# Kernel tuning notes

Measured on AMD Instinct MI355X. Metric: run time of the kernel, lower is better.

## Reference

```python
import jax, jax.numpy as jnp
import numpy as np

D_K = 64  # module-level constant in source
NEG = -1e9


def setup_inputs() -> dict:
    key = jax.random.key(0)
    k1, k2, k3, k4 = jax.random.split(key, 4)
    B, H, S, D = 4, 16, 2048, 64
    query = jax.random.normal(k1, (B, H, S, D), dtype=jnp.float32)
    key_t = jax.random.normal(k2, (B, H, S, D), dtype=jnp.float32)
    value = jax.random.normal(k3, (B, H, S, D), dtype=jnp.float32)
    mask = jax.random.randint(k4, (B, 1, S, S), 0, 2) == 1  # bool, broadcast over heads
    return {"query": query, "key": key_t, "value": value, "mask": mask}


def reference(query, key, value, mask):
    # scores = QK^T / sqrt(d_k)   [B,H,S,S]
    scores = jnp.einsum("bhqd,bhkd->bhqk", query, key) / jnp.sqrt(jnp.float32(D_K))
    # masked_fill_(mask, -1e9)
    scores = jnp.where(mask, jnp.float32(NEG), scores)
    # non-standard: multiply masked scores by V, then log_softmax over last dim
    out = jnp.einsum("bhqk,bhkd->bhqd", scores, value)  # [B,H,S,d_v]
    return jax.nn.log_softmax(out, axis=-1)
```

## Files before the change

### kernel.cpp

```cpp
#include <hip/hip_runtime.h>
#include <hip/hip_bf16.h>


typedef __attribute__((ext_vector_type(8))) short bf16x8;
typedef __attribute__((ext_vector_type(16))) float f32x16;

#define NEGV (-1e9f)

__device__ inline unsigned cvt_bf16(float f) {
    unsigned u = __builtin_bit_cast(unsigned, f);
    u += 0x7FFFu + ((u >> 16) & 1u);
    return u >> 16;
}
__device__ inline unsigned pk_bf16(float a, float b) {
    return cvt_bf16(a) | (cvt_bf16(b) << 16);
}
__device__ inline unsigned pk_trunc(float a, float b) {
    return __builtin_amdgcn_perm(__builtin_bit_cast(unsigned, b),
                                 __builtin_bit_cast(unsigned, a), 0x07060302u);
}

__global__ __launch_bounds__(256)
void mask_pack(const int* __restrict__ M, unsigned long long* __restrict__ bitT) {
    const int lane = threadIdx.x & 63;
    const int gw   = (blockIdx.x * 256 + threadIdx.x) >> 6;
    const int b    = gw >> 11;
    const int qt   = (gw >> 8) & 7;
    const int q    = gw & 255;
    const size_t mbase = (size_t)gw * 2048;
    unsigned long long* dst = bitT + (size_t)(b * 8 + qt) * 32 * 256 + q;
#pragma unroll 4
    for (int ki = 0; ki < 32; ki++) {
        const int m = M[mbase + ki * 64 + lane];
        const unsigned long long bal = __ballot(m != 0);
        if (lane == 0) dst[ki * 256] = bal;
    }
}

__global__ __launch_bounds__(256, 4)
void attn_kernel(const float* __restrict__ Q, const float* __restrict__ K,
                 const float* __restrict__ V,
                 const unsigned long long* __restrict__ bitT,
                 float* __restrict__ Out) {
    __shared__ __attribute__((aligned(16))) unsigned short sK[2][64 * 72];
    __shared__ __attribute__((aligned(16))) unsigned short sVt[2][64 * 72];

    const int tid  = threadIdx.x;
    const int wave = tid >> 6;
    const int lane = tid & 63;
    const int half = lane >> 5;
    const int l32  = lane & 31;

    const int bid = blockIdx.x;
    const int h   = bid & 15;
    const int qt2 = (bid >> 4) & 15;
    const int b   = bid >> 8;
    const int bh  = b * 16 + h;
    const int q0  = qt2 * 128;
    const int qt  = qt2 >> 1;
    const int qh  = qt2 & 1;

    const float* Qb = Q + (size_t)(bh * 2048 + q0) * 64;
    const float* Kb = K + (size_t)bh * 2048 * 64;
    const float* Vb = V + (size_t)bh * 2048 * 64;
    const unsigned long long* Bt = bitT + (size_t)(b * 8 + qt) * 32 * 256
                                 + qh * 128 + wave * 32 + l32;

    float4 kp[4];
    float  vp[16];
    unsigned long long mw = Bt[0];
    const int krow = tid >> 4, kc4 = tid & 15;
#pragma unroll
    for (int i = 0; i < 4; i++)
        kp[i] = *(const float4*)(Kb + (size_t)(krow + i * 16) * 64 + kc4 * 4);
#pragma unroll
    for (int i = 0; i < 2; i++) {
        const int kb = (wave * 2 + i) * 8;
#pragma unroll
        for (int j = 0; j < 8; j++)
            vp[i * 8 + j] = Vb[(size_t)(kb + j) * 64 + lane];
    }

    bf16x8 qF[4];
    {
        const float* qr = Qb + (size_t)(wave * 32 + l32) * 64 + half * 8;
#pragma unroll
        for (int dk = 0; dk < 4; dk++) {
            const float4 f0 = *(const float4*)(qr + dk * 16);
            const float4 f1 = *(const float4*)(qr + dk * 16 + 4);
            union { bf16x8 v; unsigned u[4]; } t;
            t.u[0] = pk_bf16(f0.x * 0.125f, f0.y * 0.125f);
            t.u[1] = pk_bf16(f0.z * 0.125f, f0.w * 0.125f);
            t.u[2] = pk_bf16(f1.x * 0.125f, f1.y * 0.125f);
            t.u[3] = pk_bf16(f1.z * 0.125f, f1.w * 0.125f);
            qF[dk] = t.v;
        }
    }

    f32x16 Oacc[2];
#pragma unroll
    for (int db = 0; db < 2; db++)
#pragma unroll
        for (int r = 0; r < 16; r++) Oacc[db][r] = 0.f;

    for (int ki = 0; ki < 32; ki++) {
        const int cur = ki & 1;

#pragma unroll
        for (int i = 0; i < 4; i++) {
            uint2 p;
            p.x = pk_trunc(kp[i].x, kp[i].y);
            p.y = pk_trunc(kp[i].z, kp[i].w);
            *(uint2*)&sK[cur][(krow + i * 16) * 72 + kc4 * 4] = p;
        }
#pragma unroll
        for (int i = 0; i < 2; i++) {
            const int kb = (wave * 2 + i) * 8;
            uint4 p4;
            p4.x = pk_trunc(vp[i * 8 + 0], vp[i * 8 + 1]);
            p4.y = pk_trunc(vp[i * 8 + 2], vp[i * 8 + 3]);
            p4.z = pk_trunc(vp[i * 8 + 4], vp[i * 8 + 5]);
            p4.w = pk_trunc(vp[i * 8 + 6], vp[i * 8 + 7]);
            *(uint4*)&sVt[cur][lane * 72 + kb] = p4;
        }

        __syncthreads();

        unsigned long long mwN = 0;
        if (ki < 31) {
            const int kn = (ki + 1) * 64;
            mwN = Bt[(ki + 1) * 256];
#pragma unroll
            for (int i = 0; i < 4; i++)
                kp[i] = *(const float4*)(Kb + (size_t)(kn + krow + i * 16) * 64 + kc4 * 4);
#pragma unroll
            for (int i = 0; i < 2; i++) {
                const int kb = (wave * 2 + i) * 8;
#pragma unroll
                for (int j = 0; j < 8; j++)
                    vp[i * 8 + j] = Vb[(size_t)(kn + kb + j) * 64 + lane];
            }
        }

#pragma unroll
        for (int jk = 0; jk < 2; jk++) {
            bf16x8 aK[4];
#pragma unroll
            for (int dk = 0; dk < 4; dk++)
                aK[dk] = *(const bf16x8*)&sK[cur][(jk * 32 + l32) * 72 + dk * 16 + half * 8];
            bf16x8 bV[2][2];
#pragma unroll
            for (int p = 0; p < 2; p++)
#pragma unroll
                for (int db = 0; db < 2; db++)
                    bV[p][db] = *(const bf16x8*)&sVt[cur][(db * 32 + l32) * 72 + (jk * 2 + p) * 16 + half * 8];

            const unsigned b32 = (unsigned)(mw >> (jk * 32));
            const unsigned bsh = b32 >> (half * 4);

            f32x16 acc;
#pragma unroll
            for (int rg = 0; rg < 4; rg++) {
                const unsigned nib = bsh >> (rg * 8);
                acc[rg * 4 + 0] = (nib & 1u) ? NEGV : 0.f;
                acc[rg * 4 + 1] = (nib & 2u) ? NEGV : 0.f;
                acc[rg * 4 + 2] = (nib & 4u) ? NEGV : 0.f;
                acc[rg * 4 + 3] = (nib & 8u) ? NEGV : 0.f;
            }
#pragma unroll
            for (int dk = 0; dk < 4; dk++)
                acc = __builtin_amdgcn_mfma_f32_32x32x16_bf16(aK[dk], qF[dk], acc, 0, 0, 0);

#pragma unroll
            for (int p = 0; p < 2; p++) {
                const unsigned P0 = pk_trunc(acc[p * 8 + 0], acc[p * 8 + 1]);
                const unsigned P1 = pk_trunc(acc[p * 8 + 2], acc[p * 8 + 3]);
                const unsigned P2 = pk_trunc(acc[p * 8 + 4], acc[p * 8 + 5]);
                const unsigned P3 = pk_trunc(acc[p * 8 + 6], acc[p * 8 + 7]);
                auto r02 = __builtin_amdgcn_permlane32_swap(P0, P2, false, false);
                auto r13 = __builtin_amdgcn_permlane32_swap(P1, P3, false, false);
                union { bf16x8 v; unsigned u[4]; } aS;
                aS.u[0] = (unsigned)r02[0];
                aS.u[1] = (unsigned)r13[0];
                aS.u[2] = (unsigned)r02[1];
                aS.u[3] = (unsigned)r13[1];
#pragma unroll
                for (int db = 0; db < 2; db++)
                    Oacc[db] = __builtin_amdgcn_mfma_f32_32x32x16_bf16(aS.v, bV[p][db], Oacc[db], 0, 0, 0);
            }
        }

        mw = mwN;
    }

    float* Ob = Out + (size_t)bh * 2048 * 64;
#pragma unroll
    for (int r = 0; r < 16; r++) {
        const float v0 = Oacc[0][r], v1 = Oacc[1][r];
        float mx = fmaxf(v0, v1);
#pragma unroll
        for (int off = 1; off < 32; off <<= 1)
            mx = fmaxf(mx, __shfl_xor(mx, off, 64));
        float s = __expf(v0 - mx) + __expf(v1 - mx);
#pragma unroll
        for (int off = 1; off < 32; off <<= 1)
            s += __shfl_xor(s, off, 64);
        const float lse = mx + __logf(s);
        const int qrow = q0 + wave * 32 + (r & 3) + 8 * (r >> 2) + 4 * half;
        Ob[(size_t)qrow * 64 + l32]      = v0 - lse;
        Ob[(size_t)qrow * 64 + 32 + l32] = v1 - lse;
    }
}

extern "C" void kernel_launch(void* const* d_in, const int* in_sizes, int n_in,
                              void* d_out, int out_size, void* d_ws, size_t ws_size,
                              hipStream_t stream) {
    const float* Q = (const float*)d_in[0];
    const float* K = (const float*)d_in[1];
    const float* V = (const float*)d_in[2];
    const int*   M = (const int*)d_in[3];
    float* Out = (float*)d_out;
    unsigned long long* bitT = (unsigned long long*)d_ws;

    mask_pack<<<dim3(2048), dim3(256), 0, stream>>>(M, bitT);
    attn_kernel<<<dim3(1024), dim3(256), 0, stream>>>(Q, K, V, bitT, Out);
}
```

Baseline: 261.5 us.

## Pre-convert K/V to swizzled bf16 and stage tiles via direct global-to-LDS loads

Adds a preconversion kernel that packs the mask bits and also converts K and transposed V to bf16 in an XOR-swizzled layout in workspace. The attention kernel then stages each tile into LDS with global_load_lds instead of loading fp32 into registers and packing in-kernel, and reads LDS with a swizzle in place of padding. This halves the bytes each of the 16 query-tile blocks per head re-reads for K/V and removes the per-iteration convert and LDS store work. The cost is an extra full pass over K and V, plus a workspace-size check that falls back to the old path.

After: 265.9 us. Within noise of the previous version (+1.7%).

```diff
diff --git a/kernel.cpp b/kernel.cpp
--- a/kernel.cpp
+++ b/kernel.cpp
@@ -18,6 +18,226 @@
 __device__ inline unsigned pk_trunc(float a, float b) {
     return __builtin_amdgcn_perm(__builtin_bit_cast(unsigned, b),
                                  __builtin_bit_cast(unsigned, a), 0x07060302u);
+}
+
+#define WS_BIT_OFF  0u
+#define WS_K_OFF    2097152u
+#define WS_V_OFF    18874368u
+#define WS_NEED     35651584ull
+
+__global__ __launch_bounds__(256)
+void preconv(const int* __restrict__ M, const float* __restrict__ K,
+             const float* __restrict__ V, unsigned long long* __restrict__ bitT,
+             unsigned short* __restrict__ Kswz, unsigned short* __restrict__ Vtswz) {
+    const int tid  = threadIdx.x;
+    const int lane = tid & 63;
+    const int wave = tid >> 6;
+    const int bid  = blockIdx.x;
+
+    if (bid < 2048) {
+        const int gw = (bid * 256 + tid) >> 6;
+        const int b  = gw >> 11;
+        const int qt = (gw >> 8) & 7;
+        const int q  = gw & 255;
+        const size_t mbase = (size_t)gw * 2048;
+        unsigned long long* dst = bitT + (size_t)(b * 8 + qt) * 32 * 256 + q;
+#pragma unroll 4
+        for (int ki = 0; ki < 32; ki++) {
+            const int m = M[mbase + ki * 64 + lane];
+            const unsigned long long bal = __ballot(m != 0);
+            if (lane == 0) dst[ki * 256] = bal;
+        }
+    } else if (bid < 6144) {
+        const unsigned g   = (unsigned)(bid - 2048) * 256 + tid;
+        const int b4  = g & 7;
+        const int row = (g >> 3) & 63;
+        const int d0  = (b4 ^ (row & 7)) * 8;
+        const float* src = K + (size_t)(g >> 3) * 64 + d0;
+        const float4 f0 = *(const float4*)(src);
+        const float4 f1 = *(const float4*)(src + 4);
+        uint4 p;
+        p.x = pk_trunc(f0.x, f0.y); p.y = pk_trunc(f0.z, f0.w);
+        p.z = pk_trunc(f1.x, f1.y); p.w = pk_trunc(f1.z, f1.w);
+        *(uint4*)&Kswz[(size_t)g * 8] = p;
+    } else {
+        const int j    = (bid - 6144) * 4 + wave;
+        const int kgrp = j & 7;
+        const int ki   = (j >> 3) & 31;
+        const int bh   = j >> 8;
+        const size_t vbase = ((size_t)(bh * 2048 + ki * 64 + kgrp * 8)) * 64 + lane;
+        float v[8];
+#pragma unroll
+        for (int jj = 0; jj < 8; jj++) v[jj] = V[vbase + jj * 64];
+        uint4 p;
+        p.x = pk_trunc(v[0], v[1]); p.y = pk_trunc(v[2], v[3]);
+        p.z = pk_trunc(v[4], v[5]); p.w = pk_trunc(v[6], v[7]);
+        const size_t chunk = ((size_t)(bh * 32 + ki) * 64 + lane) * 8 + (kgrp ^ (lane & 7));
+        *(uint4*)&Vtswz[chunk * 8] = p;
+    }
+}
+
+__global__ __launch_bounds__(256, 4)
+void attn_fast(const float* __restrict__ Q,
+               const unsigned short* __restrict__ Kswz,
+               const unsigned short* __restrict__ Vtswz,
+               const unsigned long long* __restrict__ bitT,
+               float* __restrict__ Out) {
+    __shared__ __attribute__((aligned(16))) unsigned short sK[2][64 * 64];
+    __shared__ __attribute__((aligned(16))) unsigned short sVt[2][64 * 64];
+
+    const int tid  = threadIdx.x;
+    const int wave = tid >> 6;
+    const int lane = tid & 63;
+    const int half = lane >> 5;
+    const int l32  = lane & 31;
+
+    const int bid = blockIdx.x;
+    const int h   = bid & 15;
+    const int qt2 = (bid >> 4) & 15;
+    const int b   = bid >> 8;
+    const int bh  = b * 16 + h;
+    const int q0  = qt2 * 128;
+    const int qt  = qt2 >> 1;
+    const int qh  = qt2 & 1;
+
+    const float* Qb = Q + (size_t)(bh * 2048 + q0) * 64;
+    const unsigned short* Kt = Kswz  + ((size_t)bh << 17);
+    const unsigned short* Vt = Vtswz + ((size_t)bh << 17);
+    const unsigned long long* Bt = bitT + (size_t)(b * 8 + qt) * 32 * 256
+                                 + qh * 128 + wave * 32 + l32;
+
+    #define STAGE(buf, ki) do {                                                   \
+        const unsigned short* kg_ = Kt + ((ki) << 12) + wave * 1024 + lane * 8;   \
+        const unsigned short* vg_ = Vt + ((ki) << 12) + wave * 1024 + lane * 8;   \
+        unsigned short* ks_ = &sK[buf][wave * 1024];                              \
+        unsigned short* vs_ = &sVt[buf][wave * 1024];                             \
+        __builtin_amdgcn_global_load_lds(                                         \
+            (const __attribute__((address_space(1))) void*)kg_,                   \
+            (__attribute__((address_space(3))) void*)ks_, 16, 0, 0);              \
+        __builtin_amdgcn_global_load_lds(                                         \
+            (const __attribute__((address_space(1))) void*)(kg_ + 512),           \
+            (__attribute__((address_space(3))) void*)(ks_ + 512), 16, 0, 0);      \
+        __builtin_amdgcn_global_load_lds(                                         \
+            (const __attribute__((address_space(1))) void*)vg_,                   \
+            (__attribute__((address_space(3))) void*)vs_, 16, 0, 0);              \
+        __builtin_amdgcn_global_load_lds(                                         \
+            (const __attribute__((address_space(1))) void*)(vg_ + 512),           \
+            (__attribute__((address_space(3))) void*)(vs_ + 512), 16, 0, 0);      \
+    } while (0)
+
+    STAGE(0, 0);
+    unsigned long long mw = Bt[0];
+
+    bf16x8 qF[4];
+    {
+        const float* qr = Qb + (size_t)(wave * 32 + l32) * 64 + half * 8;
+#pragma unroll
+        for (int dk = 0; dk < 4; dk++) {
+            const float4 f0 = *(const float4*)(qr + dk * 16);
+            const float4 f1 = *(const float4*)(qr + dk * 16 + 4);
+            union { bf16x8 v; unsigned u[4]; } t;
+            t.u[0] = pk_bf16(f0.x * 0.125f, f0.y * 0.125f);
+            t.u[1] = pk_bf16(f0.z * 0.125f, f0.w * 0.125f);
+            t.u[2] = pk_bf16(f1.x * 0.125f, f1.y * 0.125f);
+            t.u[3] = pk_bf16(f1.z * 0.125f, f1.w * 0.125f);
+            qF[dk] = t.v;
+        }
+    }
+
+    f32x16 Oacc[2];
+#pragma unroll
+    for (int db = 0; db < 2; db++)
+#pragma unroll
+        for (int r = 0; r < 16; r++) Oacc[db][r] = 0.f;
+
+    __syncthreads();
+
+    const int swz = (l32 & 7) << 4;
+
+    for (int ki = 0; ki < 32; ki++) {
+        const int cur = ki & 1;
+
+        unsigned long long mwN = 0;
+        if (ki < 31) {
+            STAGE(cur ^ 1, ki + 1);
+            mwN = Bt[(ki + 1) * 256];
+        }
+
+        const char* sKc = (const char*)sK[cur];
+        const char* sVc = (const char*)sVt[cur];
+
+#pragma unroll
+        for (int jk = 0; jk < 2; jk++) {
+            bf16x8 aK[4];
+#pragma unroll
+            for (int dk = 0; dk < 4; dk++)
+                aK[dk] = *(const bf16x8*)(sKc +
+                    ((((jk * 32 + l32) * 128) + dk * 32 + half * 16) ^ swz));
+            bf16x8 bV[2][2];
+#pragma unroll
+            for (int p = 0; p < 2; p++)
+#pragma unroll
+                for (int db = 0; db < 2; db++)
+                    bV[p][db] = *(const bf16x8*)(sVc +
+                        ((((db * 32 + l32) * 128) + (jk * 2 + p) * 32 + half * 16) ^ swz));
+
+            const unsigned b32 = (unsigned)(mw >> (jk * 32));
+            const unsigned bsh = b32 >> (half * 4);
+
+            f32x16 acc;
+#pragma unroll
+            for (int rg = 0; rg < 4; rg++) {
+                const unsigned nib = bsh >> (rg * 8);
+                acc[rg * 4 + 0] = (nib & 1u) ? NEGV : 0.f;
+                acc[rg * 4 + 1] = (nib & 2u) ? NEGV : 0.f;
+                acc[rg * 4 + 2] = (nib & 4u) ? NEGV : 0.f;
+                acc[rg * 4 + 3] = (nib & 8u) ? NEGV : 0.f;
+            }
+#pragma unroll
+            for (int dk = 0; dk < 4; dk++)
+                acc = __builtin_amdgcn_mfma_f32_32x32x16_bf16(aK[dk], qF[dk], acc, 0, 0, 0);
+
+#pragma unroll
+            for (int p = 0; p < 2; p++) {
+                const unsigned P0 = pk_trunc(acc[p * 8 + 0], acc[p * 8 + 1]);
+                const unsigned P1 = pk_trunc(acc[p * 8 + 2], acc[p * 8 + 3]);
+                const unsigned P2 = pk_trunc(acc[p * 8 + 4], acc[p * 8 + 5]);
+                const unsigned P3 = pk_trunc(acc[p * 8 + 6], acc[p * 8 + 7]);
+                auto r02 = __builtin_amdgcn_permlane32_swap(P0, P2, false, false);
+                auto r13 = __builtin_amdgcn_permlane32_swap(P1, P3, false, false);
+                union { bf16x8 v; unsigned u[4]; } aS;
+                aS.u[0] = (unsigned)r02[0];
+                aS.u[1] = (unsigned)r13[0];
+                aS.u[2] = (unsigned)r02[1];
+                aS.u[3] = (unsigned)r13[1];
+#pragma unroll
+                for (int db = 0; db < 2; db++)
+                    Oacc[db] = __builtin_amdgcn_mfma_f32_32x32x16_bf16(aS.v, bV[p][db], Oacc[db], 0, 0, 0);
+            }
+        }
+
+        mw = mwN;
+        __syncthreads();
+    }
+
+    float* Ob = Out + (size_t)bh * 2048 * 64;
+#pragma unroll
+    for (int r = 0; r < 16; r++) {
+        const float v0 = Oacc[0][r], v1 = Oacc[1][r];
+        float mx = fmaxf(v0, v1);
+#pragma unroll
+        for (int off = 1; off < 32; off <<= 1)
+            mx = fmaxf(mx, __shfl_xor(mx, off, 64));
+        float s = __expf(v0 - mx) + __expf(v1 - mx);
+#pragma unroll
+        for (int off = 1; off < 32; off <<= 1)
+            s += __shfl_xor(s, off, 64);
+        const float lse = mx + __logf(s);
+        const int qrow = q0 + wave * 32 + (r & 3) + 8 * (r >> 2) + 4 * half;
+        Ob[(size_t)qrow * 64 + l32]      = v0 - lse;
+        Ob[(size_t)qrow * 64 + 32 + l32] = v1 - lse;
+    }
+    #undef STAGE
 }
 
 __global__ __launch_bounds__(256)
@@ -38,10 +258,10 @@
 }
 
 __global__ __launch_bounds__(256, 4)
-void attn_kernel(const float* __restrict__ Q, const float* __restrict__ K,
-                 const float* __restrict__ V,
-                 const unsigned long long* __restrict__ bitT,
-                 float* __restrict__ Out) {
+void attn_v10(const float* __restrict__ Q, const float* __restrict__ K,
+              const float* __restrict__ V,
+              const unsigned long long* __restrict__ bitT,
+              float* __restrict__ Out) {
     __shared__ __attribute__((aligned(16))) unsigned short sK[2][64 * 72];
     __shared__ __attribute__((aligned(16))) unsigned short sVt[2][64 * 72];
 
@@ -105,7 +325,6 @@
 
     for (int ki = 0; ki < 32; ki++) {
         const int cur = ki & 1;
-
 #pragma unroll
         for (int i = 0; i < 4; i++) {
             uint2 p;
@@ -222,6 +441,13 @@
     float* Out = (float*)d_out;
     unsigned long long* bitT = (unsigned long long*)d_ws;
 
-    mask_pack<<<dim3(2048), dim3(256), 0, stream>>>(M, bitT);
-    attn_kernel<<<dim3(1024), dim3(256), 0, stream>>>(Q, K, V, bitT, Out);
-}
+    if (ws_size >= WS_NEED) {
+        unsigned short* Kswz  = (unsigned short*)((char*)d_ws + WS_K_OFF);
+        unsigned short* Vtswz = (unsigned short*)((char*)d_ws + WS_V_OFF);
+        preconv<<<dim3(10240), dim3(256), 0, stream>>>(M, K, V, bitT, Kswz, Vtswz);
+        attn_fast<<<dim3(1024), dim3(256), 0, stream>>>(Q, Kswz, Vtswz, bitT, Out);
+    } else {
+        mask_pack<<<dim3(2048), dim3(256), 0, stream>>>(M, bitT);
+        attn_v10<<<dim3(1024), dim3(256), 0, stream>>>(Q, K, V, bitT, Out);
+    }
+}
```
